# Optimization experiments

Measured on AMD Instinct MI355X. Metric: run time of the kernel, lower is better.

Reference implementation:

```python
import jax, jax.numpy as jnp
import numpy as np

K = 9          # kernel taps along the space-filling curve
SIGMA = 1.0    # gaussian bandwidth (conv2 uses SIGMA * stride, stride=1)
EPS = 1e-5     # BatchNorm eps


def _weighted_conv(x, w, coords, indices, reindices, sigma):
    """Gather points into curve order, run a k-tap 1D conv whose taps are
    modulated by a Gaussian of coordinate distance, scatter back.
    x: [B,C,N], w: [O,C,K], coords: [B,3,N], indices/reindices: [B,N]."""
    B, C, N = x.shape
    pad = K // 2
    idx = indices[:, None, :]
    xp = jnp.take_along_axis(x, jnp.broadcast_to(idx, (B, C, N)), axis=2)        # curve order
    cp = jnp.take_along_axis(coords, jnp.broadcast_to(idx, (B, 3, N)), axis=2)
    x_pad = jnp.pad(xp, ((0, 0), (0, 0), (pad, pad)))
    c_pad = jnp.pad(cp, ((0, 0), (0, 0), (pad, pad)))
    inv_s2 = 1.0 / (sigma * sigma)
    out = jnp.zeros((B, w.shape[0], N), x.dtype)
    for t in range(K):  # small fixed loop over kernel taps
        xw = x_pad[:, :, t:t + N]                     # [B,C,N]
        rel = c_pad[:, :, t:t + N] - cp               # [B,3,N]
        g = jnp.exp(-jnp.sum(rel * rel, axis=1) * inv_s2)  # [B,N] gaussian weight
        out = out + jnp.einsum('oc,bcn->bon', w[:, :, t], xw * g[:, None, :])
    ridx = reindices[:, None, :]
    return jnp.take_along_axis(out, jnp.broadcast_to(ridx, out.shape), axis=2)


def _batchnorm1d(x, gamma, beta):
    # training-mode BN over (batch, points) per channel, biased variance
    mean = jnp.mean(x, axis=(0, 2), keepdims=True)
    var = jnp.mean((x - mean) ** 2, axis=(0, 2), keepdims=True)
    return gamma[None, :, None] * (x - mean) * jax.lax.rsqrt(var + EPS) + beta[None, :, None]


def setup_inputs() -> dict:
    key = jax.random.key(0)
    ks = jax.random.split(key, 6)
    B, C, N = 4, 128, 65536
    x = jax.random.normal(ks[0], (B, C, N), jnp.float32)
    coords = jax.random.uniform(ks[1], (B, 3, N), jnp.float32)
    perm = jnp.stack([jax.random.permutation(jax.random.fold_in(ks[2], b), N) for b in range(B)])
    indices = perm.astype(jnp.int32)
    reindices = jnp.argsort(perm, axis=1).astype(jnp.int32)
    w1 = jax.random.normal(ks[3], (C, C, K), jnp.float32) * 0.05
    w2 = jax.random.normal(ks[4], (C, C, K), jnp.float32) * 0.05
    gamma1 = jnp.ones((C,), jnp.float32)
    beta1 = jnp.zeros((C,), jnp.float32)
    gamma2 = jnp.ones((C,), jnp.float32)
    beta2 = jnp.zeros((C,), jnp.float32)
    return {"x": x, "coords": coords, "indices": indices, "reindices": reindices,
            "w1": w1, "gamma1": gamma1, "beta1": beta1,
            "w2": w2, "gamma2": gamma2, "beta2": beta2}


def reference(x, coords, indices, reindices, w1, gamma1, beta1, w2, gamma2, beta2):
    identity = x
    out = _weighted_conv(x, w1, coords, indices, reindices, SIGMA)
    out = jax.nn.relu(_batchnorm1d(out, gamma1, beta1))
    out = _weighted_conv(out, w2, coords, indices, reindices, SIGMA * 1)  # stride=1
    out = _batchnorm1d(out, gamma2, beta2)
    return jax.nn.relu(out + identity)
```

## Files before the change

### kernel.cpp

```cpp
#include <hip/hip_runtime.h>

#define Bn 4
#define Cn 128
#define Nn 65536
#define KT 9
#define T_OUT 256
#define T_HALO 264
#define XROW 136
#define GROW 264

typedef _Float16 f16x8 __attribute__((ext_vector_type(8)));
typedef _Float16 f16x4 __attribute__((ext_vector_type(4)));
typedef float f32x4 __attribute__((ext_vector_type(4)));

__global__ __launch_bounds__(256) void repack_w(const float* __restrict__ w1,
                                                const float* __restrict__ w2,
                                                _Float16* __restrict__ Wr) {
  int i = blockIdx.x * 256 + threadIdx.x;
  int c = i & 127;
  int o = (i >> 7) & 127;
  int t = (i >> 14) % KT;
  int cv = i / (KT << 14);
  const float* w = cv ? w2 : w1;
  Wr[i] = (_Float16)w[(o * 128 + c) * KT + t];
}

__global__ __launch_bounds__(256) void gather_x(const float* __restrict__ x,
                                                const int* __restrict__ reidx,
                                                _Float16* __restrict__ xp) {
  __shared__ __align__(16) _Float16 tile[64 * XROW];
  int tid = threadIdx.x;
  int b = blockIdx.x >> 10;
  int n0 = (blockIdx.x & 1023) * 64;
  int j = tid & 63;
  int cw = tid >> 6;
  const float* xb = x + (size_t)b * Cn * Nn;
  for (int ci = 0; ci < 32; ++ci) {
    int c = ci * 4 + cw;
    float v = xb[(size_t)c * Nn + n0 + j];
    tile[j * XROW + c] = (_Float16)v;
  }
  __syncthreads();
  int ch = tid & 15;
#pragma unroll
  for (int pass = 0; pass < 4; ++pass) {
    int r = pass * 16 + (tid >> 4);
    int m = reidx[(size_t)b * Nn + n0 + r];
    f16x8 v = *(const f16x8*)(&tile[r * XROW + ch * 8]);
    *(f16x8*)(xp + ((size_t)b * Nn + m) * Cn + ch * 8) = v;
  }
}

__global__ __launch_bounds__(256) void gather_cp(const float* __restrict__ coords,
                                                 const int* __restrict__ indices,
                                                 float* __restrict__ cp) {
  int gidx = blockIdx.x * 256 + threadIdx.x;
  int b = gidx >> 16;
  int m = gidx & (Nn - 1);
  int idx = indices[gidx];
  const float* cb = coords + (size_t)b * 3 * Nn;
  float* cpb = cp + (size_t)b * 3 * Nn;
  cpb[m] = cb[idx];
  cpb[Nn + m] = cb[Nn + idx];
  cpb[2 * Nn + m] = cb[2 * Nn + idx];
}

__global__ __launch_bounds__(256) void compute_g(const float* __restrict__ cp,
                                                 float* __restrict__ G) {
  int gidx = blockIdx.x * 256 + threadIdx.x;
  int b = gidx >> 16;
  int m = gidx & (Nn - 1);
  const float* cpb = cp + (size_t)b * 3 * Nn;
  float x0 = cpb[m], y0 = cpb[Nn + m], z0 = cpb[2 * Nn + m];
  float* Gb = G + (size_t)b * KT * Nn;
#pragma unroll
  for (int t = 0; t < KT; ++t) {
    int q = m + t - 4;
    q = q < 0 ? 0 : (q > Nn - 1 ? Nn - 1 : q);
    float dx = cpb[q] - x0;
    float dy = cpb[Nn + q] - y0;
    float dz = cpb[2 * Nn + q] - z0;
    Gb[(size_t)t * Nn + m] = __expf(-(dx * dx + dy * dy + dz * dz));
  }
}

__global__ void bncoeff(const float* __restrict__ sums,
                        const float* __restrict__ gamma,
                        const float* __restrict__ beta,
                        float* __restrict__ coeff) {
  int c = threadIdx.x;
  const float inv = 1.0f / (float)((size_t)Bn * Nn);
  float mean = sums[c] * inv;
  float var = sums[128 + c] * inv - mean * mean;
  float a = gamma[c] * rsqrtf(var + 1e-5f);
  coeff[c] = a;
  coeff[128 + c] = beta[c] - mean * a;
}

__device__ __forceinline__ f16x8 scale8(f16x8 v, _Float16 g) {
  f16x8 r;
#pragma unroll
  for (int i = 0; i < 8; ++i) r[i] = v[i] * g;
  return r;
}

template <int TRANS>
__global__ __launch_bounds__(256) void conv_mfma(
    const _Float16* __restrict__ Xin, const _Float16* __restrict__ W,
    const float* __restrict__ G, _Float16* __restrict__ Yout,
    float* __restrict__ sums, const float* __restrict__ coeff) {
  __shared__ __align__(16) _Float16 Xs[T_HALO * XROW];
  __shared__ __align__(4) _Float16 Gs[KT * GROW];
  __shared__ float red[512];

  const int tid = threadIdx.x;
  const int b = blockIdx.x >> 8;
  const int p0 = (blockIdx.x & 255) * T_OUT;
  const int ch = tid & 15;

  float ca[8], cb[8];
  if (TRANS) {
#pragma unroll
    for (int i = 0; i < 8; ++i) {
      ca[i] = coeff[ch * 8 + i];
      cb[i] = coeff[128 + ch * 8 + i];
    }
  }
#pragma unroll
  for (int pass = 0; pass < 17; ++pass) {
    int r = pass * 16 + (tid >> 4);
    if (r < T_HALO) {
      int q = p0 - 4 + r;
      f16x8 v = {0, 0, 0, 0, 0, 0, 0, 0};
      if (q >= 0 && q < Nn) {
        v = *(const f16x8*)(Xin + ((size_t)b * Nn + q) * Cn + ch * 8);
        if (TRANS) {
#pragma unroll
          for (int i = 0; i < 8; ++i) {
            float f = fmaxf(ca[i] * (float)v[i] + cb[i], 0.f);
            v[i] = (_Float16)f;
          }
        }
      }
      *(f16x8*)(&Xs[r * XROW + ch * 8]) = v;
    }
  }
  {
    const float* gb = G + (size_t)b * KT * Nn + p0;
    for (int i = tid; i < KT * 256; i += 256) {
      int t = i >> 8;
      int p = i & 255;
      Gs[t * GROW + p] = (_Float16)gb[(size_t)t * Nn + p];
    }
  }

  const int w = tid >> 6;
  const int lane = tid & 63;
  const int l15 = lane & 15;
  const int quad = lane >> 4;
  const int wm = w >> 1;
  const int wn = w & 1;

  f32x4 acc[4][8];
  const f32x4 z4 = {0.f, 0.f, 0.f, 0.f};
#pragma unroll
  for (int mt = 0; mt < 4; ++mt)
#pragma unroll
    for (int nt = 0; nt < 8; ++nt) acc[mt][nt] = z4;

  __syncthreads();

#pragma unroll 1
  for (int t = 0; t < KT; ++t) {
    _Float16 gt[8];
#pragma unroll
    for (int nt = 0; nt < 8; ++nt)
      gt[nt] = Gs[t * GROW + wn * 128 + nt * 16 + l15];

    const _Float16* Wt = W + ((size_t)t << 14) + (wm * 64) * Cn;
#pragma unroll
    for (int ko = 0; ko < 4; ++ko) {
      f16x8 a[4];
#pragma unroll
      for (int mt = 0; mt < 4; ++mt)
        a[mt] = *(const f16x8*)(Wt + (mt * 16 + l15) * Cn + ko * 32 + quad * 8);
#pragma unroll
      for (int nt = 0; nt < 8; ++nt) {
        f16x8 bv = *(const f16x8*)(&Xs[(wn * 128 + nt * 16 + l15 + t) * XROW + ko * 32 + quad * 8]);
        bv = scale8(bv, gt[nt]);
#pragma unroll
        for (int mt = 0; mt < 4; ++mt)
          acc[mt][nt] = __builtin_amdgcn_mfma_f32_16x16x32_f16(a[mt], bv, acc[mt][nt], 0, 0, 0);
      }
    }
  }

  f32x4 s4[4], q4[4];
#pragma unroll
  for (int mt = 0; mt < 4; ++mt) {
#pragma unroll
    for (int rg = 0; rg < 4; ++rg) {
      float s = 0.f, q = 0.f;
#pragma unroll
      for (int nt = 0; nt < 8; ++nt) {
        float v = acc[mt][nt][rg];
        s += v;
        q += v * v;
      }
#pragma unroll
      for (int m = 1; m < 16; m <<= 1) {
        s += __shfl_xor(s, m);
        q += __shfl_xor(q, m);
      }
      s4[mt][rg] = s;
      q4[mt][rg] = q;
    }
  }
  __syncthreads();
  if (l15 == 0) {
#pragma unroll
    for (int mt = 0; mt < 4; ++mt) {
      int cbase = wm * 64 + mt * 16 + quad * 4;
      *(f32x4*)(&red[wn * 128 + cbase]) = s4[mt];
      *(f32x4*)(&red[256 + wn * 128 + cbase]) = q4[mt];
    }
  }

  _Float16* Os = Xs;
#pragma unroll
  for (int mt = 0; mt < 4; ++mt)
#pragma unroll
    for (int nt = 0; nt < 8; ++nt) {
      f16x4 o4;
#pragma unroll
      for (int rg = 0; rg < 4; ++rg) o4[rg] = (_Float16)acc[mt][nt][rg];
      *(f16x4*)(&Os[(wn * 128 + nt * 16 + l15) * XROW + wm * 64 + mt * 16 + quad * 4]) = o4;
    }
  __syncthreads();

  if (tid < 128) {
    atomicAdd(&sums[tid], red[tid] + red[128 + tid]);
    atomicAdd(&sums[128 + tid], red[256 + tid] + red[384 + tid]);
  }
#pragma unroll
  for (int pass = 0; pass < 16; ++pass) {
    int r = pass * 16 + (tid >> 4);
    f16x8 v = *(const f16x8*)(&Os[r * XROW + ch * 8]);
    *(f16x8*)(Yout + ((size_t)b * Nn + p0 + r) * Cn + ch * 8) = v;
  }
}

__global__ __launch_bounds__(256) void final_k(const _Float16* __restrict__ y2,
                                               const float* __restrict__ x,
                                               const int* __restrict__ reidx,
                                               const float* __restrict__ coeff,
                                               float* __restrict__ out) {
  __shared__ __align__(16) _Float16 tile[64 * XROW];
  __shared__ float Ac[128], Bc[128];
  int tid = threadIdx.x;
  int b = blockIdx.x >> 10;
  int n0 = (blockIdx.x & 1023) * 64;
  if (tid < 128) {
    Ac[tid] = coeff[tid];
    Bc[tid] = coeff[128 + tid];
  }
  int ch = tid & 15;
#pragma unroll
  for (int pass = 0; pass < 4; ++pass) {
    int r = pass * 16 + (tid >> 4);
    int m = reidx[(size_t)b * Nn + n0 + r];
    f16x8 v = *(const f16x8*)(y2 + ((size_t)b * Nn + m) * Cn + ch * 8);
    *(f16x8*)(&tile[r * XROW + ch * 8]) = v;
  }
  __syncthreads();
  int j = tid & 63;
  int cw = tid >> 6;
  for (int ci = 0; ci < 32; ++ci) {
    int c = ci * 4 + cw;
    float v = (float)tile[j * XROW + c];
    size_t gi = ((size_t)b * Cn + c) * Nn + n0 + j;
    float r = Ac[c] * v + Bc[c] + x[gi];
    out[gi] = fmaxf(r, 0.f);
  }
}

extern "C" void kernel_launch(void* const* d_in, const int* in_sizes, int n_in,
                              void* d_out, int out_size, void* d_ws, size_t ws_size,
                              hipStream_t stream) {
  (void)in_sizes; (void)n_in; (void)out_size; (void)ws_size;
  const float* x = (const float*)d_in[0];
  const float* coords = (const float*)d_in[1];
  const int* indices = (const int*)d_in[2];
  const int* reindices = (const int*)d_in[3];
  const float* w1 = (const float*)d_in[4];
  const float* gamma1 = (const float*)d_in[5];
  const float* beta1 = (const float*)d_in[6];
  const float* w2 = (const float*)d_in[7];
  const float* gamma2 = (const float*)d_in[8];
  const float* beta2 = (const float*)d_in[9];
  float* out = (float*)d_out;

  char* ws = (char*)d_ws;
  const size_t BUF0 = (size_t)Bn * Nn * Cn * sizeof(_Float16);
  _Float16* buf0 = (_Float16*)ws;
  float* sums1 = (float*)(ws + BUF0);
  float* sums2 = sums1 + 256;
  float* coeff1 = sums1 + 512;
  float* coeff2 = sums1 + 768;
  _Float16* Wr = (_Float16*)(ws + BUF0 + 4096);

  char* dob = (char*)d_out;
  _Float16* y1 = (_Float16*)dob;
  float* cp = (float*)(dob + BUF0);
  float* G = (float*)(dob + BUF0 + (size_t)Bn * 3 * Nn * 4);

  hipMemsetAsync(sums1, 0, 512 * sizeof(float), stream);

  repack_w<<<1152, 256, 0, stream>>>(w1, w2, Wr);
  gather_x<<<Bn * 1024, 256, 0, stream>>>(x, reindices, buf0);
  gather_cp<<<1024, 256, 0, stream>>>(coords, indices, cp);
  compute_g<<<1024, 256, 0, stream>>>(cp, G);

  conv_mfma<0><<<Bn * 256, 256, 0, stream>>>(buf0, Wr, G, y1, sums1, nullptr);
  bncoeff<<<1, 128, 0, stream>>>(sums1, gamma1, beta1, coeff1);
  conv_mfma<1><<<Bn * 256, 256, 0, stream>>>(y1, Wr + (size_t)KT * Cn * Cn, G,
                                             buf0, sums2, coeff1);
  bncoeff<<<1, 128, 0, stream>>>(sums2, gamma2, beta2, coeff2);
  final_k<<<Bn * 1024, 256, 0, stream>>>(buf0, x, reindices, coeff2, out);
}
```

Measured before the change: 581.3 us.

## Vectorize transpose kernels via fp32 LDS tile and shrink conv LDS for occupancy

gather_x and final_k now move the channel-major fp32 tensors with 16-byte vector loads and stores through a padded fp32 shared tile, replacing scalar per-element accesses. The transpose is done on the LDS side with strided scalar reads or writes. conv_mfma aliases the gaussian weight buffer with the reduction buffer and requests two blocks per CU through launch bounds. It also drops the per-thread coefficient registers, reading coeff from global memory instead. The aim is better global-memory coalescing and higher occupancy, at the risk of LDS bank conflicts and register spills under the tighter bound.

Result: faster. 562.2 us (-3.3%).

```diff
diff --git a/kernel.cpp b/kernel.cpp
--- a/kernel.cpp
+++ b/kernel.cpp
@@ -8,10 +8,12 @@
 #define T_HALO 264
 #define XROW 136
 #define GROW 264
+#define FT 66
 
 typedef _Float16 f16x8 __attribute__((ext_vector_type(8)));
 typedef _Float16 f16x4 __attribute__((ext_vector_type(4)));
 typedef float f32x4 __attribute__((ext_vector_type(4)));
+typedef float f32x2 __attribute__((ext_vector_type(2)));
 
 __global__ __launch_bounds__(256) void repack_w(const float* __restrict__ w1,
                                                 const float* __restrict__ w2,
@@ -28,25 +30,32 @@
 __global__ __launch_bounds__(256) void gather_x(const float* __restrict__ x,
                                                 const int* __restrict__ reidx,
                                                 _Float16* __restrict__ xp) {
-  __shared__ __align__(16) _Float16 tile[64 * XROW];
+  __shared__ float ft[128 * FT];
   int tid = threadIdx.x;
   int b = blockIdx.x >> 10;
   int n0 = (blockIdx.x & 1023) * 64;
-  int j = tid & 63;
-  int cw = tid >> 6;
   const float* xb = x + (size_t)b * Cn * Nn;
-  for (int ci = 0; ci < 32; ++ci) {
-    int c = ci * 4 + cw;
-    float v = xb[(size_t)c * Nn + n0 + j];
-    tile[j * XROW + c] = (_Float16)v;
+  {
+    int cc = tid >> 4;
+    int j4 = (tid & 15) * 4;
+#pragma unroll
+    for (int pass = 0; pass < 8; ++pass) {
+      int c = pass * 16 + cc;
+      f32x4 v = *(const f32x4*)(&xb[(size_t)c * Nn + n0 + j4]);
+      *(f32x2*)(&ft[c * FT + j4]) = f32x2{v.x, v.y};
+      *(f32x2*)(&ft[c * FT + j4 + 2]) = f32x2{v.z, v.w};
+    }
   }
   __syncthreads();
   int ch = tid & 15;
+  int rr = tid >> 4;
 #pragma unroll
   for (int pass = 0; pass < 4; ++pass) {
-    int r = pass * 16 + (tid >> 4);
+    int r = pass * 16 + rr;
     int m = reidx[(size_t)b * Nn + n0 + r];
-    f16x8 v = *(const f16x8*)(&tile[r * XROW + ch * 8]);
+    f16x8 v;
+#pragma unroll
+    for (int k = 0; k < 8; ++k) v[k] = (_Float16)ft[(ch * 8 + k) * FT + r];
     *(f16x8*)(xp + ((size_t)b * Nn + m) * Cn + ch * 8) = v;
   }
 }
@@ -105,27 +114,20 @@
 }
 
 template <int TRANS>
-__global__ __launch_bounds__(256) void conv_mfma(
+__global__ __launch_bounds__(256, 2) void conv_mfma(
     const _Float16* __restrict__ Xin, const _Float16* __restrict__ W,
     const float* __restrict__ G, _Float16* __restrict__ Yout,
     float* __restrict__ sums, const float* __restrict__ coeff) {
   __shared__ __align__(16) _Float16 Xs[T_HALO * XROW];
-  __shared__ __align__(4) _Float16 Gs[KT * GROW];
-  __shared__ float red[512];
+  __shared__ __align__(16) unsigned char aux[KT * GROW * 2];
+  _Float16* Gs = (_Float16*)aux;
+  float* red = (float*)aux;
 
   const int tid = threadIdx.x;
   const int b = blockIdx.x >> 8;
   const int p0 = (blockIdx.x & 255) * T_OUT;
   const int ch = tid & 15;
 
-  float ca[8], cb[8];
-  if (TRANS) {
-#pragma unroll
-    for (int i = 0; i < 8; ++i) {
-      ca[i] = coeff[ch * 8 + i];
-      cb[i] = coeff[128 + ch * 8 + i];
-    }
-  }
 #pragma unroll
   for (int pass = 0; pass < 17; ++pass) {
     int r = pass * 16 + (tid >> 4);
@@ -137,7 +139,7 @@
         if (TRANS) {
 #pragma unroll
           for (int i = 0; i < 8; ++i) {
-            float f = fmaxf(ca[i] * (float)v[i] + cb[i], 0.f);
+            float f = fmaxf(coeff[ch * 8 + i] * (float)v[i] + coeff[128 + ch * 8 + i], 0.f);
             v[i] = (_Float16)f;
           }
         }
@@ -255,32 +257,39 @@
                                                const int* __restrict__ reidx,
                                                const float* __restrict__ coeff,
                                                float* __restrict__ out) {
-  __shared__ __align__(16) _Float16 tile[64 * XROW];
-  __shared__ float Ac[128], Bc[128];
+  __shared__ float ft[128 * FT];
   int tid = threadIdx.x;
   int b = blockIdx.x >> 10;
   int n0 = (blockIdx.x & 1023) * 64;
-  if (tid < 128) {
-    Ac[tid] = coeff[tid];
-    Bc[tid] = coeff[128 + tid];
-  }
-  int ch = tid & 15;
-#pragma unroll
-  for (int pass = 0; pass < 4; ++pass) {
-    int r = pass * 16 + (tid >> 4);
-    int m = reidx[(size_t)b * Nn + n0 + r];
-    f16x8 v = *(const f16x8*)(y2 + ((size_t)b * Nn + m) * Cn + ch * 8);
-    *(f16x8*)(&tile[r * XROW + ch * 8]) = v;
-  }
-  __syncthreads();
-  int j = tid & 63;
-  int cw = tid >> 6;
-  for (int ci = 0; ci < 32; ++ci) {
-    int c = ci * 4 + cw;
-    float v = (float)tile[j * XROW + c];
-    size_t gi = ((size_t)b * Cn + c) * Nn + n0 + j;
-    float r = Ac[c] * v + Bc[c] + x[gi];
-    out[gi] = fmaxf(r, 0.f);
+  {
+    int ch = tid & 15;
+#pragma unroll
+    for (int pass = 0; pass < 4; ++pass) {
+      int r = pass * 16 + (tid >> 4);
+      int m = reidx[(size_t)b * Nn + n0 + r];
+      f16x8 v = *(const f16x8*)(y2 + ((size_t)b * Nn + m) * Cn + ch * 8);
+#pragma unroll
+      for (int k = 0; k < 8; ++k) ft[(ch * 8 + k) * FT + r] = (float)v[k];
+    }
+  }
+  __syncthreads();
+  int cc = tid >> 4;
+  int j4 = (tid & 15) * 4;
+#pragma unroll
+  for (int pass = 0; pass < 8; ++pass) {
+    int c = pass * 16 + cc;
+    float a = coeff[c];
+    float bb = coeff[128 + c];
+    f32x2 v0 = *(const f32x2*)(&ft[c * FT + j4]);
+    f32x2 v1 = *(const f32x2*)(&ft[c * FT + j4 + 2]);
+    size_t gi = ((size_t)b * Cn + c) * Nn + n0 + j4;
+    f32x4 xv = *(const f32x4*)(&x[gi]);
+    f32x4 r;
+    r.x = fmaxf(a * v0.x + bb + xv.x, 0.f);
+    r.y = fmaxf(a * v0.y + bb + xv.y, 0.f);
+    r.z = fmaxf(a * v1.x + bb + xv.z, 0.f);
+    r.w = fmaxf(a * v1.y + bb + xv.w, 0.f);
+    *(f32x4*)(&out[gi]) = r;
   }
 }
 
```
